# Performance work log

Measured on AMD Instinct MI355X. Metric: run time of the kernel, lower is better.

## Reference

```python
import jax, jax.numpy as jnp
import numpy as np

N_UPDATE = 3

def _lin(key, fan_in, fan_out):
    s = 1.0 / np.sqrt(fan_in)
    k1, k2 = jax.random.split(key)
    W = jax.random.uniform(k1, (fan_in, fan_out), jnp.float32, -s, s)
    b = jax.random.uniform(k2, (fan_out,), jnp.float32, -s, s)
    return W, b

def setup_inputs() -> dict:
    key = jax.random.key(0)
    ks = jax.random.split(key, 12)
    N, E, F_NODE, F_EDGE, H, L, R, T = 50000, 400000, 16, 16, 32, 64, 128, 1
    inp = {}
    inp["x"] = jax.random.normal(ks[0], (N, F_NODE), jnp.float32)
    inp["edge_index"] = jax.random.randint(ks[1], (E, 2), 0, N)  # [E,2] (src,dst)
    inp["edge_attr"] = jax.random.normal(ks[2], (E, F_EDGE), jnp.float32)
    # edge MLP: F_EDGE -> 64 -> 64 -> H*H
    inp["Wm0"], inp["bm0"] = _lin(ks[3], F_EDGE, L)
    inp["Wm1"], inp["bm1"] = _lin(ks[4], L, L)
    inp["Wm2"], inp["bm2"] = _lin(ks[5], L, H * H)
    # NNConv root weight + bias
    inp["root"], inp["bias"] = _lin(ks[6], H, H)
    # readout i-net: 2H -> R -> T ; j-net: H -> R -> T
    inp["Wi0"], inp["bi0"] = _lin(ks[7], 2 * H, R)
    inp["Wi1"], inp["bi1"] = _lin(ks[8], R, T)
    inp["Wj0"], inp["bj0"] = _lin(ks[9], H, R)
    inp["Wj1"], inp["bj1"] = _lin(ks[10], R, T)
    return inp

def reference(x, edge_index, edge_attr, Wm0, bm0, Wm1, bm1, Wm2, bm2,
              root, bias, Wi0, bi0, Wi1, bi1, Wj0, bj0, Wj1, bj1):
    N = x.shape[0]
    H = root.shape[0]
    # h_0 = [x, zeros] padded to hidden_state_size
    h0 = jnp.concatenate([x, jnp.zeros((N, H - x.shape[1]), x.dtype)], axis=1)
    # edge MLP -> per-edge weight matrices (edge_attr constant across updates)
    e = jax.nn.relu(edge_attr @ Wm0 + bm0)
    e = jax.nn.relu(e @ Wm1 + bm1)
    W = (e @ Wm2 + bm2).reshape(-1, H, H)  # [E, H, H]
    src = edge_index[:, 0]
    dst = edge_index[:, 1]
    h = h0
    for _ in range(N_UPDATE):
        msg = jnp.einsum('eh,eho->eo', h[src], W)              # gather + bmm
        agg = jax.ops.segment_sum(msg, dst, num_segments=N)    # scatter-add
        h = h @ root + bias + agg                              # NNConv root/bias
    # mpnn readout: sum_v sigmoid(i([h_T, h_0])) * j(h_T)
    gate = jax.nn.sigmoid(jax.nn.relu(jnp.concatenate([h, h0], 1) @ Wi0 + bi0) @ Wi1 + bi1)
    val = jax.nn.relu(h @ Wj0 + bj0) @ Wj1 + bj1
    return jnp.sum(gate * val, axis=0)  # [target_size]
```

## Files before the change

### kernel.cpp

```cpp
#include <hip/hip_runtime.h>
#include <stdint.h>

#define N_UPDATE 3
#define HD 32
#define FN 16

typedef unsigned short u16;
typedef __bf16 bf16x8 __attribute__((ext_vector_type(8)));
typedef float f32x4 __attribute__((ext_vector_type(4)));

__device__ __forceinline__ float bf2f(u16 u) {
  union { uint32_t i; float f; } v; v.i = ((uint32_t)u) << 16; return v.f;
}
__device__ __forceinline__ u16 f2bf(float f) {
  union { uint32_t i; float f; } v; v.f = f;
  uint32_t x = v.i;
  return (u16)((x + 0x7fffu + ((x >> 16) & 1u)) >> 16);
}

union frag16 { uint4 v; bf16x8 b; u16 s[8]; };

__global__ void k_zero(float* __restrict__ p, int n) {
  int i = blockIdx.x * blockDim.x + threadIdx.x;
  if (i < n) p[i] = 0.f;
}

__global__ void k_prep_bf(const float* __restrict__ Wm2, uint4* __restrict__ Bf) {
  int t = blockIdx.x;
  int lane = threadIdx.x;
  int col = lane & 15;
  int hg = lane >> 4;
  frag16 f;
#pragma unroll
  for (int jj = 0; jj < 8; jj++) {
    int h = hg * 8 + jj;
    int j = t * 16 + col;
    int kk = j & 63;
    int o = j >> 6;
    f.s[jj] = f2bf(Wm2[kk * 1024 + h * 32 + o]);
  }
  Bf[t * 64 + lane] = f.v;
}

__global__ void k_init_h(const float* __restrict__ x, float* __restrict__ h, int N) {
  int idx = blockIdx.x * blockDim.x + threadIdx.x;
  if (idx >= N * HD) return;
  int n = idx >> 5, c = idx & 31;
  h[idx] = (c < FN) ? x[n * FN + c] : 0.f;
}

__global__ __launch_bounds__(256) void k_edge_mlp(
    const float* __restrict__ ea,
    const float* __restrict__ Wm0, const float* __restrict__ bm0,
    const float* __restrict__ Wm1, const float* __restrict__ bm1,
    u16* __restrict__ ee, int E) {
  int e = blockIdx.x * blockDim.x + threadIdx.x;
  if (e >= E) return;
  float a[16];
  {
    const float4* p = (const float4*)(ea + (size_t)e * 16);
    float4 v0 = p[0], v1 = p[1], v2 = p[2], v3 = p[3];
    a[0]=v0.x; a[1]=v0.y; a[2]=v0.z; a[3]=v0.w;
    a[4]=v1.x; a[5]=v1.y; a[6]=v1.z; a[7]=v1.w;
    a[8]=v2.x; a[9]=v2.y; a[10]=v2.z; a[11]=v2.w;
    a[12]=v3.x; a[13]=v3.y; a[14]=v3.z; a[15]=v3.w;
  }
  float t0[64];
#pragma unroll
  for (int j = 0; j < 64; j++) t0[j] = bm0[j];
#pragma unroll
  for (int k = 0; k < 16; k++) {
    float av = a[k];
#pragma unroll
    for (int j = 0; j < 64; j++) t0[j] = fmaf(av, Wm0[k * 64 + j], t0[j]);
  }
#pragma unroll
  for (int j = 0; j < 64; j++) t0[j] = fmaxf(t0[j], 0.f);

#pragma unroll
  for (int half = 0; half < 2; half++) {
    float t1[32];
#pragma unroll
    for (int j = 0; j < 32; j++) t1[j] = bm1[half * 32 + j];
#pragma unroll
    for (int k = 0; k < 64; k++) {
      float tv = t0[k];
#pragma unroll
      for (int j = 0; j < 32; j++) t1[j] = fmaf(tv, Wm1[k * 64 + half * 32 + j], t1[j]);
    }
    unsigned int out[16];
#pragma unroll
    for (int j = 0; j < 16; j++) {
      u16 lo = f2bf(fmaxf(t1[2 * j], 0.f));
      u16 hi = f2bf(fmaxf(t1[2 * j + 1], 0.f));
      out[j] = (unsigned int)lo | ((unsigned int)hi << 16);
    }
    uint4* op = (uint4*)(ee + (size_t)e * 64 + half * 32);
#pragma unroll
    for (int q = 0; q < 4; q++) {
      uint4 w; w.x = out[q*4+0]; w.y = out[q*4+1]; w.z = out[q*4+2]; w.w = out[q*4+3];
      op[q] = w;
    }
  }
}

__global__ __launch_bounds__(256) void k_hb(
    const float* __restrict__ h, const float* __restrict__ bm2,
    float* __restrict__ hb, int N) {
  int t = blockIdx.x * blockDim.x + threadIdx.x;
  int n = t >> 5, o = t & 31;
  if (n >= N) return;
  float hv = h[(size_t)n * HD + o];
  float acc = 0.f;
#pragma unroll
  for (int k = 0; k < 32; k++)
    acc = fmaf(__shfl(hv, k, 32), bm2[k * 32 + o], acc);
  hb[(size_t)n * HD + o] = acc;
}

__global__ __launch_bounds__(256) void k_gemm_G(
    const float* __restrict__ h, const uint4* __restrict__ Bf,
    u16* __restrict__ Gb, int N, int o_base, int OC) {
  int wave = threadIdx.x >> 6;
  int lane = threadIdx.x & 63;
  int jt = o_base * 4 + blockIdx.y * 4 + wave;
  int n0 = blockIdx.x * 16;
  int row = lane & 15;
  int kg = lane >> 4;

  int nr = n0 + row; if (nr > N - 1) nr = N - 1;
  const float* hr = h + (size_t)nr * HD + kg * 8;
  float4 f0 = *(const float4*)hr;
  float4 f1 = *(const float4*)(hr + 4);
  frag16 a;
  a.s[0] = f2bf(f0.x); a.s[1] = f2bf(f0.y); a.s[2] = f2bf(f0.z); a.s[3] = f2bf(f0.w);
  a.s[4] = f2bf(f1.x); a.s[5] = f2bf(f1.y); a.s[6] = f2bf(f1.z); a.s[7] = f2bf(f1.w);

  frag16 b; b.v = Bf[jt * 64 + lane];

  f32x4 acc = {0.f, 0.f, 0.f, 0.f};
  acc = __builtin_amdgcn_mfma_f32_16x16x32_bf16(a.b, b.b, acc, 0, 0, 0);

  int j = jt * 16 + row;
  int o_l = (j >> 6) - o_base;
  int k = j & 63;
#pragma unroll
  for (int r = 0; r < 4; r++) {
    int n = n0 + kg * 4 + r;
    if (n < N) Gb[((size_t)n * OC + o_l) * 64 + k] = f2bf(acc[r]);
  }
}

__global__ __launch_bounds__(256) void k_msg(
    const u16* __restrict__ Gb, const float* __restrict__ hb,
    const u16* __restrict__ ee, const int* __restrict__ eidx,
    float* __restrict__ agg, int E, int o_base, int ocShift) {
  int t = blockIdx.x * blockDim.x + threadIdx.x;
  int e = t >> ocShift;
  int o_l = t & ((1 << ocShift) - 1);
  if (e >= E) return;
  const int2 sd = ((const int2*)eidx)[e];
  int o = o_base + o_l;

  float acc = hb[(size_t)sd.x * HD + o];

  const uint4* ep = (const uint4*)(ee + (size_t)e * 64);
  const uint4* gp = (const uint4*)(Gb + (((size_t)sd.x << ocShift) + o_l) * 64);
  frag16 eu[8], gu[8];
#pragma unroll
  for (int q = 0; q < 8; q++) { eu[q].v = ep[q]; gu[q].v = gp[q]; }
#pragma unroll
  for (int k = 0; k < 64; k++) {
    acc = fmaf(bf2f(eu[k >> 3].s[k & 7]), bf2f(gu[k >> 3].s[k & 7]), acc);
  }
  atomicAdd(&agg[(size_t)sd.y * HD + o], acc);
}

__global__ __launch_bounds__(256) void k_update(
    const float* __restrict__ h, const float* __restrict__ agg,
    const float* __restrict__ root, const float* __restrict__ bias,
    float* __restrict__ hn, int N) {
  int t = blockIdx.x * blockDim.x + threadIdx.x;
  int n = t >> 5, o = t & 31;
  if (n >= N) return;
  float hv = h[(size_t)n * HD + o];
  float acc = bias[o] + agg[(size_t)n * HD + o];
#pragma unroll
  for (int k = 0; k < 32; k++)
    acc = fmaf(__shfl(hv, k, 32), root[k * HD + o], acc);
  hn[(size_t)n * HD + o] = acc;
}

__global__ __launch_bounds__(256) void k_readout(
    const float* __restrict__ h, const float* __restrict__ x,
    const float* __restrict__ Wi0, const float* __restrict__ bi0,
    const float* __restrict__ Wi1, const float* __restrict__ bi1,
    const float* __restrict__ Wj0, const float* __restrict__ bj0,
    const float* __restrict__ Wj1, const float* __restrict__ bj1,
    float* __restrict__ partial, int N) {
  int wid = threadIdx.x >> 6;
  int lane = threadIdx.x & 63;
  int n = blockIdx.x * 4 + wid;
  __shared__ float sred[4];
  float contrib = 0.f;
  if (n < N) {
    float uv;
    if (lane < 32) uv = h[(size_t)n * HD + lane];
    else if (lane < 48) uv = x[(size_t)n * FN + lane - 32];
    else uv = 0.f;

    float g1a = bi0[lane], g1b = bi0[lane + 64];
#pragma unroll
    for (int k = 0; k < 64; k++) {
      float u = __shfl(uv, k, 64);
      g1a = fmaf(u, Wi0[k * 128 + lane], g1a);
      g1b = fmaf(u, Wi0[k * 128 + lane + 64], g1b);
    }
    g1a = fmaxf(g1a, 0.f); g1b = fmaxf(g1b, 0.f);
    float gp = g1a * Wi1[lane] + g1b * Wi1[lane + 64];

    float v1a = bj0[lane], v1b = bj0[lane + 64];
#pragma unroll
    for (int k = 0; k < 32; k++) {
      float hk = __shfl(uv, k, 64);
      v1a = fmaf(hk, Wj0[k * 128 + lane], v1a);
      v1b = fmaf(hk, Wj0[k * 128 + lane + 64], v1b);
    }
    v1a = fmaxf(v1a, 0.f); v1b = fmaxf(v1b, 0.f);
    float vp = v1a * Wj1[lane] + v1b * Wj1[lane + 64];

#pragma unroll
    for (int s = 32; s; s >>= 1) {
      gp += __shfl_xor(gp, s, 64);
      vp += __shfl_xor(vp, s, 64);
    }
    float gate = 1.f / (1.f + __expf(-(gp + bi1[0])));
    float val = vp + bj1[0];
    contrib = gate * val;
  }
  if (lane == 0) sred[wid] = contrib;
  __syncthreads();
  if (threadIdx.x == 0) partial[blockIdx.x] = sred[0] + sred[1] + sred[2] + sred[3];
}

__global__ void k_final(const float* __restrict__ partial, float* __restrict__ out, int P) {
  __shared__ float sm[256];
  float s = 0.f;
  for (int i = threadIdx.x; i < P; i += 256) s += partial[i];
  sm[threadIdx.x] = s;
  __syncthreads();
  for (int st = 128; st; st >>= 1) {
    if ((int)threadIdx.x < st) sm[threadIdx.x] += sm[threadIdx.x + st];
    __syncthreads();
  }
  if (threadIdx.x == 0) out[0] = sm[0];
}

extern "C" void kernel_launch(void* const* d_in, const int* in_sizes, int n_in,
                              void* d_out, int out_size, void* d_ws, size_t ws_size,
                              hipStream_t stream) {
  const float* x    = (const float*)d_in[0];
  const int*   eidx = (const int*)d_in[1];
  const float* ea   = (const float*)d_in[2];
  const float* Wm0  = (const float*)d_in[3];
  const float* bm0  = (const float*)d_in[4];
  const float* Wm1  = (const float*)d_in[5];
  const float* bm1  = (const float*)d_in[6];
  const float* Wm2  = (const float*)d_in[7];
  const float* bm2  = (const float*)d_in[8];
  const float* root = (const float*)d_in[9];
  const float* bias = (const float*)d_in[10];
  const float* Wi0  = (const float*)d_in[11];
  const float* bi0  = (const float*)d_in[12];
  const float* Wi1  = (const float*)d_in[13];
  const float* bi1  = (const float*)d_in[14];
  const float* Wj0  = (const float*)d_in[15];
  const float* bj0  = (const float*)d_in[16];
  const float* Wj1  = (const float*)d_in[17];
  const float* bj1  = (const float*)d_in[18];

  int N = in_sizes[0] / FN;
  int E = in_sizes[1] / 2;
  int nb = (N + 3) / 4;

  auto al = [](size_t b) { return (b + 255) & ~(size_t)255; };
  size_t ee_b = al((size_t)E * 64 * 2);
  size_t bf_b = al(128 * 64 * sizeof(uint4));
  size_t nv_b = al((size_t)N * HD * 4);
  size_t pa_b = al((size_t)nb * 4);
  size_t fixed = ee_b + bf_b + 4 * nv_b + pa_b;

  int OC = 0, ocShift = 0;
  for (int c = 32, s = 5; c >= 4; c >>= 1, s--) {
    size_t gb_b = al((size_t)N * c * 64 * 2);
    if (fixed + gb_b <= ws_size) { OC = c; ocShift = s; break; }
  }
  if (OC == 0) return;

  char* ws = (char*)d_ws;
  size_t off = 0;
  auto alloc = [&](size_t bytes) { void* p = ws + off; off += al(bytes); return p; };
  u16*   Gb      = (u16*)alloc((size_t)N * OC * 64 * 2);
  u16*   ee      = (u16*)alloc((size_t)E * 64 * 2);
  uint4* Bf      = (uint4*)alloc(128 * 64 * sizeof(uint4));
  float* hb      = (float*)alloc((size_t)N * HD * 4);
  float* hA      = (float*)alloc((size_t)N * HD * 4);
  float* hB      = (float*)alloc((size_t)N * HD * 4);
  float* agg     = (float*)alloc((size_t)N * HD * 4);
  float* partial = (float*)alloc((size_t)nb * 4);

  int mt = (N + 15) / 16;
  int nwarp_grid = (N * HD + 255) / 256;

  hipLaunchKernelGGL(k_prep_bf, dim3(128), dim3(64), 0, stream, Wm2, Bf);
  hipLaunchKernelGGL(k_init_h, dim3(nwarp_grid), dim3(256), 0, stream, x, hA, N);
  hipLaunchKernelGGL(k_edge_mlp, dim3((E + 255) / 256), dim3(256), 0, stream,
                     ea, Wm0, bm0, Wm1, bm1, ee, E);

  float* hc = hA; float* hn = hB;
  for (int it = 0; it < N_UPDATE; it++) {
    hipLaunchKernelGGL(k_zero, dim3(nwarp_grid), dim3(256), 0, stream, agg, N * HD);
    hipLaunchKernelGGL(k_hb, dim3(nwarp_grid), dim3(256), 0, stream, hc, bm2, hb, N);
    for (int ob = 0; ob < HD; ob += OC) {
      hipLaunchKernelGGL(k_gemm_G, dim3(mt, OC), dim3(256), 0, stream, hc, Bf, Gb, N, ob, OC);
      hipLaunchKernelGGL(k_msg, dim3(((size_t)E * OC + 255) / 256), dim3(256), 0, stream,
                         Gb, hb, ee, eidx, agg, E, ob, ocShift);
    }
    hipLaunchKernelGGL(k_update, dim3(nwarp_grid), dim3(256), 0, stream,
                       hc, agg, root, bias, hn, N);
    float* tmp = hc; hc = hn; hn = tmp;
  }

  hipLaunchKernelGGL(k_readout, dim3(nb), dim3(256), 0, stream,
                     hc, x, Wi0, bi0, Wi1, bi1, Wj0, bj0, Wj1, bj1, partial, N);
  hipLaunchKernelGGL(k_final, dim3(1), dim3(256), 0, stream, partial, (float*)d_out, nb);
}
```

Before: 1.549 ms.

## Sort edges by source and process outputs in two fixed halves

```diff
diff --git a/kernel.cpp b/kernel.cpp
--- a/kernel.cpp
+++ b/kernel.cpp
@@ -20,9 +20,51 @@
 
 union frag16 { uint4 v; bf16x8 b; u16 s[8]; };
 
-__global__ void k_zero(float* __restrict__ p, int n) {
+__global__ void k_zero_f(float* __restrict__ p, int n) {
   int i = blockIdx.x * blockDim.x + threadIdx.x;
   if (i < n) p[i] = 0.f;
+}
+__global__ void k_zero_i(int* __restrict__ p, int n) {
+  int i = blockIdx.x * blockDim.x + threadIdx.x;
+  if (i < n) p[i] = 0;
+}
+
+__global__ void k_hist(const int* __restrict__ eidx, int* __restrict__ cnt, int E) {
+  int e = blockIdx.x * blockDim.x + threadIdx.x;
+  if (e >= E) return;
+  atomicAdd(&cnt[eidx[2 * e]], 1);
+}
+
+__global__ __launch_bounds__(1024) void k_scan(const int* __restrict__ cnt,
+                                               int* __restrict__ ptr, int N) {
+  __shared__ int sums[1024];
+  int chunk = (N + 1023) / 1024;
+  int beg = threadIdx.x * chunk;
+  int end = beg + chunk; if (end > N) end = N;
+  int s = 0;
+  for (int i = beg; i < end; i++) s += cnt[i];
+  sums[threadIdx.x] = s;
+  __syncthreads();
+  for (int off = 1; off < 1024; off <<= 1) {
+    int v = (threadIdx.x >= off) ? sums[threadIdx.x - off] : 0;
+    __syncthreads();
+    sums[threadIdx.x] += v;
+    __syncthreads();
+  }
+  int run = (threadIdx.x == 0) ? 0 : sums[threadIdx.x - 1];
+  for (int i = beg; i < end; i++) { ptr[i] = run; run += cnt[i]; }
+}
+
+__global__ void k_scatter(const int* __restrict__ eidx, int* __restrict__ ptr,
+                          int* __restrict__ se_src, int* __restrict__ se_dst,
+                          int* __restrict__ invp, int E) {
+  int e = blockIdx.x * blockDim.x + threadIdx.x;
+  if (e >= E) return;
+  int2 sd = ((const int2*)eidx)[e];
+  int pos = atomicAdd(&ptr[sd.x], 1);
+  se_src[pos] = sd.x;
+  se_dst[pos] = sd.y;
+  invp[e] = pos;
 }
 
 __global__ void k_prep_bf(const float* __restrict__ Wm2, uint4* __restrict__ Bf) {
@@ -30,14 +72,16 @@
   int lane = threadIdx.x;
   int col = lane & 15;
   int hg = lane >> 4;
+  int p = t >> 6;
+  int t2 = t & 63;
+  int j2 = t2 * 16 + col;
+  int o = p * 16 + (j2 >> 6);
+  int k = j2 & 63;
   frag16 f;
 #pragma unroll
   for (int jj = 0; jj < 8; jj++) {
     int h = hg * 8 + jj;
-    int j = t * 16 + col;
-    int kk = j & 63;
-    int o = j >> 6;
-    f.s[jj] = f2bf(Wm2[kk * 1024 + h * 32 + o]);
+    f.s[jj] = f2bf(Wm2[k * 1024 + h * 32 + o]);
   }
   Bf[t * 64 + lane] = f.v;
 }
@@ -53,7 +97,7 @@
     const float* __restrict__ ea,
     const float* __restrict__ Wm0, const float* __restrict__ bm0,
     const float* __restrict__ Wm1, const float* __restrict__ bm1,
-    u16* __restrict__ ee, int E) {
+    const int* __restrict__ invp, u16* __restrict__ ee, int E) {
   int e = blockIdx.x * blockDim.x + threadIdx.x;
   if (e >= E) return;
   float a[16];
@@ -77,6 +121,7 @@
 #pragma unroll
   for (int j = 0; j < 64; j++) t0[j] = fmaxf(t0[j], 0.f);
 
+  u16* dst = ee + (size_t)invp[e] * 64;
 #pragma unroll
   for (int half = 0; half < 2; half++) {
     float t1[32];
@@ -95,7 +140,7 @@
       u16 hi = f2bf(fmaxf(t1[2 * j + 1], 0.f));
       out[j] = (unsigned int)lo | ((unsigned int)hi << 16);
     }
-    uint4* op = (uint4*)(ee + (size_t)e * 64 + half * 32);
+    uint4* op = (uint4*)(dst + half * 32);
 #pragma unroll
     for (int q = 0; q < 4; q++) {
       uint4 w; w.x = out[q*4+0]; w.y = out[q*4+1]; w.z = out[q*4+2]; w.w = out[q*4+3];
@@ -104,26 +149,12 @@
   }
 }
 
-__global__ __launch_bounds__(256) void k_hb(
-    const float* __restrict__ h, const float* __restrict__ bm2,
-    float* __restrict__ hb, int N) {
-  int t = blockIdx.x * blockDim.x + threadIdx.x;
-  int n = t >> 5, o = t & 31;
-  if (n >= N) return;
-  float hv = h[(size_t)n * HD + o];
-  float acc = 0.f;
-#pragma unroll
-  for (int k = 0; k < 32; k++)
-    acc = fmaf(__shfl(hv, k, 32), bm2[k * 32 + o], acc);
-  hb[(size_t)n * HD + o] = acc;
-}
-
 __global__ __launch_bounds__(256) void k_gemm_G(
     const float* __restrict__ h, const uint4* __restrict__ Bf,
-    u16* __restrict__ Gb, int N, int o_base, int OC) {
+    u16* __restrict__ Gb, int N, int p) {
   int wave = threadIdx.x >> 6;
   int lane = threadIdx.x & 63;
-  int jt = o_base * 4 + blockIdx.y * 4 + wave;
+  int jt = blockIdx.y * 4 + wave;
   int n0 = blockIdx.x * 16;
   int row = lane & 15;
   int kg = lane >> 4;
@@ -136,36 +167,43 @@
   a.s[0] = f2bf(f0.x); a.s[1] = f2bf(f0.y); a.s[2] = f2bf(f0.z); a.s[3] = f2bf(f0.w);
   a.s[4] = f2bf(f1.x); a.s[5] = f2bf(f1.y); a.s[6] = f2bf(f1.z); a.s[7] = f2bf(f1.w);
 
-  frag16 b; b.v = Bf[jt * 64 + lane];
+  frag16 b; b.v = Bf[(p * 64 + jt) * 64 + lane];
 
   f32x4 acc = {0.f, 0.f, 0.f, 0.f};
   acc = __builtin_amdgcn_mfma_f32_16x16x32_bf16(a.b, b.b, acc, 0, 0, 0);
 
-  int j = jt * 16 + row;
-  int o_l = (j >> 6) - o_base;
-  int k = j & 63;
+  int j2 = jt * 16 + row;
 #pragma unroll
   for (int r = 0; r < 4; r++) {
     int n = n0 + kg * 4 + r;
-    if (n < N) Gb[((size_t)n * OC + o_l) * 64 + k] = f2bf(acc[r]);
+    if (n < N) Gb[(size_t)n * 1024 + j2] = f2bf(acc[r]);
   }
 }
 
 __global__ __launch_bounds__(256) void k_msg(
-    const u16* __restrict__ Gb, const float* __restrict__ hb,
-    const u16* __restrict__ ee, const int* __restrict__ eidx,
-    float* __restrict__ agg, int E, int o_base, int ocShift) {
+    const u16* __restrict__ Gb, const float* __restrict__ h,
+    const float* __restrict__ bm2, const u16* __restrict__ ee,
+    const int* __restrict__ se_src, const int* __restrict__ se_dst,
+    float* __restrict__ agg, int E, int p) {
   int t = blockIdx.x * blockDim.x + threadIdx.x;
-  int e = t >> ocShift;
-  int o_l = t & ((1 << ocShift) - 1);
+  int e = t >> 4;
+  int o_l = t & 15;
   if (e >= E) return;
-  const int2 sd = ((const int2*)eidx)[e];
-  int o = o_base + o_l;
-
-  float acc = hb[(size_t)sd.x * HD + o];
+  int src = se_src[e];
+  int dst = se_dst[e];
+  int o = p * 16 + o_l;
+
+  float hv0 = h[(size_t)src * HD + o_l];
+  float hv1 = h[(size_t)src * HD + 16 + o_l];
+  float acc = 0.f;
+#pragma unroll
+  for (int hh = 0; hh < 16; hh++) {
+    acc = fmaf(__shfl(hv0, hh, 16), bm2[hh * 32 + o], acc);
+    acc = fmaf(__shfl(hv1, hh, 16), bm2[(hh + 16) * 32 + o], acc);
+  }
 
   const uint4* ep = (const uint4*)(ee + (size_t)e * 64);
-  const uint4* gp = (const uint4*)(Gb + (((size_t)sd.x << ocShift) + o_l) * 64);
+  const uint4* gp = (const uint4*)(Gb + ((size_t)src * 16 + o_l) * 64);
   frag16 eu[8], gu[8];
 #pragma unroll
   for (int q = 0; q < 8; q++) { eu[q].v = ep[q]; gu[q].v = gp[q]; }
@@ -173,11 +211,11 @@
   for (int k = 0; k < 64; k++) {
     acc = fmaf(bf2f(eu[k >> 3].s[k & 7]), bf2f(gu[k >> 3].s[k & 7]), acc);
   }
-  atomicAdd(&agg[(size_t)sd.y * HD + o], acc);
+  atomicAdd(&agg[(size_t)dst * HD + o], acc);
 }
 
 __global__ __launch_bounds__(256) void k_update(
-    const float* __restrict__ h, const float* __restrict__ agg,
+    const float* __restrict__ h, float* __restrict__ agg,
     const float* __restrict__ root, const float* __restrict__ bias,
     float* __restrict__ hn, int N) {
   int t = blockIdx.x * blockDim.x + threadIdx.x;
@@ -185,6 +223,7 @@
   if (n >= N) return;
   float hv = h[(size_t)n * HD + o];
   float acc = bias[o] + agg[(size_t)n * HD + o];
+  agg[(size_t)n * HD + o] = 0.f;
 #pragma unroll
   for (int k = 0; k < 32; k++)
     acc = fmaf(__shfl(hv, k, 32), root[k * HD + o], acc);
@@ -284,49 +323,50 @@
   int nb = (N + 3) / 4;
 
   auto al = [](size_t b) { return (b + 255) & ~(size_t)255; };
-  size_t ee_b = al((size_t)E * 64 * 2);
-  size_t bf_b = al(128 * 64 * sizeof(uint4));
-  size_t nv_b = al((size_t)N * HD * 4);
-  size_t pa_b = al((size_t)nb * 4);
-  size_t fixed = ee_b + bf_b + 4 * nv_b + pa_b;
-
-  int OC = 0, ocShift = 0;
-  for (int c = 32, s = 5; c >= 4; c >>= 1, s--) {
-    size_t gb_b = al((size_t)N * c * 64 * 2);
-    if (fixed + gb_b <= ws_size) { OC = c; ocShift = s; break; }
-  }
-  if (OC == 0) return;
+  size_t need = al((size_t)N * 1024 * 2) + al((size_t)E * 64 * 2) +
+                al(128 * 64 * sizeof(uint4)) + 3 * al((size_t)N * HD * 4) +
+                2 * al((size_t)N * 4) + 3 * al((size_t)E * 4) + al((size_t)nb * 4);
+  if (need > ws_size) return;
 
   char* ws = (char*)d_ws;
   size_t off = 0;
   auto alloc = [&](size_t bytes) { void* p = ws + off; off += al(bytes); return p; };
-  u16*   Gb      = (u16*)alloc((size_t)N * OC * 64 * 2);
+  u16*   Gb      = (u16*)alloc((size_t)N * 1024 * 2);
   u16*   ee      = (u16*)alloc((size_t)E * 64 * 2);
   uint4* Bf      = (uint4*)alloc(128 * 64 * sizeof(uint4));
-  float* hb      = (float*)alloc((size_t)N * HD * 4);
   float* hA      = (float*)alloc((size_t)N * HD * 4);
   float* hB      = (float*)alloc((size_t)N * HD * 4);
   float* agg     = (float*)alloc((size_t)N * HD * 4);
+  int*   cnt     = (int*)alloc((size_t)N * 4);
+  int*   ptr     = (int*)alloc((size_t)N * 4);
+  int*   se_src  = (int*)alloc((size_t)E * 4);
+  int*   se_dst  = (int*)alloc((size_t)E * 4);
+  int*   invp    = (int*)alloc((size_t)E * 4);
   float* partial = (float*)alloc((size_t)nb * 4);
 
   int mt = (N + 15) / 16;
-  int nwarp_grid = (N * HD + 255) / 256;
+  int ng = (N * HD + 255) / 256;
+  int eg = (E + 255) / 256;
+
+  hipLaunchKernelGGL(k_zero_i, dim3((N + 255) / 256), dim3(256), 0, stream, cnt, N);
+  hipLaunchKernelGGL(k_hist, dim3(eg), dim3(256), 0, stream, eidx, cnt, E);
+  hipLaunchKernelGGL(k_scan, dim3(1), dim3(1024), 0, stream, cnt, ptr, N);
+  hipLaunchKernelGGL(k_scatter, dim3(eg), dim3(256), 0, stream, eidx, ptr, se_src, se_dst, invp, E);
 
   hipLaunchKernelGGL(k_prep_bf, dim3(128), dim3(64), 0, stream, Wm2, Bf);
-  hipLaunchKernelGGL(k_init_h, dim3(nwarp_grid), dim3(256), 0, stream, x, hA, N);
-  hipLaunchKernelGGL(k_edge_mlp, dim3((E + 255) / 256), dim3(256), 0, stream,
-                     ea, Wm0, bm0, Wm1, bm1, ee, E);
+  hipLaunchKernelGGL(k_init_h, dim3(ng), dim3(256), 0, stream, x, hA, N);
+  hipLaunchKernelGGL(k_edge_mlp, dim3(eg), dim3(256), 0, stream,
+                     ea, Wm0, bm0, Wm1, bm1, invp, ee, E);
+  hipLaunchKernelGGL(k_zero_f, dim3(ng), dim3(256), 0, stream, agg, N * HD);
 
   float* hc = hA; float* hn = hB;
   for (int it = 0; it < N_UPDATE; it++) {
-    hipLaunchKernelGGL(k_zero, dim3(nwarp_grid), dim3(256), 0, stream, agg, N * HD);
-    hipLaunchKernelGGL(k_hb, dim3(nwarp_grid), dim3(256), 0, stream, hc, bm2, hb, N);
-    for (int ob = 0; ob < HD; ob += OC) {
-      hipLaunchKernelGGL(k_gemm_G, dim3(mt, OC), dim3(256), 0, stream, hc, Bf, Gb, N, ob, OC);
-      hipLaunchKernelGGL(k_msg, dim3(((size_t)E * OC + 255) / 256), dim3(256), 0, stream,
-                         Gb, hb, ee, eidx, agg, E, ob, ocShift);
-    }
-    hipLaunchKernelGGL(k_update, dim3(nwarp_grid), dim3(256), 0, stream,
+    for (int p = 0; p < 2; p++) {
+      hipLaunchKernelGGL(k_gemm_G, dim3(mt, 16), dim3(256), 0, stream, hc, Bf, Gb, N, p);
+      hipLaunchKernelGGL(k_msg, dim3(((size_t)E * 16 + 255) / 256), dim3(256), 0, stream,
+                         Gb, hc, bm2, ee, se_src, se_dst, agg, E, p);
+    }
+    hipLaunchKernelGGL(k_update, dim3(ng), dim3(256), 0, stream,
                        hc, agg, root, bias, hn, N);
     float* tmp = hc; hc = hn; hn = tmp;
   }
```

Result: slower. 1.607 ms (+3.8%).
